# Optimization experiments

Hardware: AMD Instinct MI355X
Metric: run time of the kernel (lower is better)

The kernel has to match this reference:

```python
import jax, jax.numpy as jnp
import numpy as np

N_NODES = 100000
N_EDGES = 2000000


def _init_mlp(key, dims, scale=0.05):
    Ws, bs = [], []
    ks = jax.random.split(key, len(dims) - 1)
    for k, di, do in zip(ks, dims[:-1], dims[1:]):
        Ws.append(jax.random.normal(k, (di, do), dtype=jnp.float32) * scale)
        bs.append(jnp.zeros((do,), dtype=jnp.float32))
    return Ws, bs


def setup_inputs() -> dict:
    key = jax.random.key(0)
    ks = jax.random.split(key, 7)
    d = {
        "t": jax.random.uniform(ks[0], (1,), dtype=jnp.float32),
        "x": jax.random.normal(ks[1], (N_NODES, 4), dtype=jnp.float32),
        "Ofixed": jax.random.normal(ks[2], (N_NODES, 2), dtype=jnp.float32),
        "src_idx": jax.random.randint(ks[3], (N_EDGES,), 0, N_NODES, dtype=jnp.int32),
        "tgt_idx": jax.random.randint(ks[4], (N_EDGES,), 0, N_NODES, dtype=jnp.int32),
    }
    # fR: (2*d_O+1)=13 -> [150]*4 -> 50 ; fO: 50 -> [100] -> 4
    R_Ws, R_bs = _init_mlp(ks[5], [13, 150, 150, 150, 150, 50])
    O_Ws, O_bs = _init_mlp(ks[6], [50, 100, 4])
    for i, (W, b) in enumerate(zip(R_Ws, R_bs)):
        d[f"fR_W{i}"] = W
        d[f"fR_b{i}"] = b
    for i, (W, b) in enumerate(zip(O_Ws, O_bs)):
        d[f"fO_W{i}"] = W
        d[f"fO_b{i}"] = b
    return d


def _mlp(h, Ws, bs):
    # hidden layers with ReLU, linear output (matches MLP in the torch code)
    for W, b in zip(Ws[:-1], bs[:-1]):
        h = jax.nn.relu(h @ W + b)
    return h @ Ws[-1] + bs[-1]


def reference(t, x, Ofixed, src_idx, tgt_idx,
              fR_W0, fR_b0, fR_W1, fR_b1, fR_W2, fR_b2, fR_W3, fR_b3, fR_W4, fR_b4,
              fO_W0, fO_b0, fO_W1, fO_b1):
    O = jnp.concatenate([x, Ofixed], axis=1)            # [N, d_O]
    # Msrc.T @ O and Mtgt.T @ O with 0/1 incidence matrices == gathers
    Rsrc = O[src_idx]                                   # [M, d_O]
    Rtgt = O[tgt_idx]                                   # [M, d_O]
    tt = jnp.broadcast_to(t.reshape(1, 1).astype(O.dtype), (src_idx.shape[0], 1))
    R_prime = jnp.concatenate([Rsrc, Rtgt, tt], axis=1)  # [M, 2*d_O+1]
    E = _mlp(R_prime, [fR_W0, fR_W1, fR_W2, fR_W3, fR_W4],
             [fR_b0, fR_b1, fR_b2, fR_b3, fR_b4])        # [M, d_E]
    # Mtgt @ E == scatter-add of edge messages onto target nodes
    E_prime = jax.ops.segment_sum(E, tgt_idx, num_segments=x.shape[0])  # [N, d_E]
    P = _mlp(E_prime, [fO_W0, fO_W1], [fO_b0, fO_b1])    # [N, d_P]
    return P
```

## Files before the change

kernel.cpp:

```cpp
#include <hip/hip_runtime.h>
#include <hip/hip_bf16.h>

typedef unsigned short u16;
typedef __attribute__((ext_vector_type(8))) short short8;
typedef __attribute__((ext_vector_type(4))) float f32x4;

constexpr int SA     = 168;
constexpr int BLK_E  = 64;
constexpr int NTHR   = 256;
constexpr int CHUNK  = 512;
constexpr int WSLOT  = 50 * CHUNK;
constexpr size_t WT_BYTES = 5ull * WSLOT * 2;
constexpr size_t WS_HDR   = 262144;

constexpr int Ls (int s) { return s == 0 ? 0 : (s <= 15 ? 1 + (s - 1) / 5 : 4); }
constexpr int Kss(int s) { return s == 0 ? 0 : (s <= 15 ? (s - 1) % 5 : s - 16); }

__device__ __forceinline__ u16 f2bf(float f) {
    union { float f; unsigned u; } c; c.f = f;
    return (u16)((c.u + 0x7fffu + ((c.u >> 16) & 1u)) >> 16);
}
__device__ __forceinline__ unsigned pk_bf16(float a, float b) {
    float2 f; f.x = a; f.y = b;
    __hip_bfloat162 h = __float22bfloat162_rn(f);
    return *(unsigned*)&h;
}

__device__ __forceinline__ int kperm(int kp) {
    if (kp < 64)  return (kp & 3) * 16 + (kp >> 2);
    if (kp < 128) { const int m = kp - 64; return (5 + (m & 3)) * 16 + (m >> 2); }
    if (kp < 144) return 4 * 16 + (kp - 128);
    if (kp < 160) return 9 * 16 + (kp - 144);
    return 1 << 30;
}

__global__ void prep_all(const float* __restrict__ W0, const float* __restrict__ W1,
                         const float* __restrict__ W2, const float* __restrict__ W3,
                         const float* __restrict__ W4,
                         const float* __restrict__ B0, const float* __restrict__ B1,
                         const float* __restrict__ B2, const float* __restrict__ B3,
                         const float* __restrict__ B4,
                         u16* __restrict__ Wt)
{
    const int l = blockIdx.y;
    const float* W; const float* B; int DI, DO; bool perm;
    if      (l == 0) { W = W0; B = B0; DI = 13;  DO = 150; perm = false; }
    else if (l == 1) { W = W1; B = B1; DI = 150; DO = 150; perm = true;  }
    else if (l == 2) { W = W2; B = B2; DI = 150; DO = 150; perm = true;  }
    else if (l == 3) { W = W3; B = B3; DI = 150; DO = 150; perm = true;  }
    else             { W = W4; B = B4; DI = 150; DO = 50;  perm = true;  }
    const int kbias = (l == 0) ? 13 : 150;
    u16* dst = Wt + (size_t)l * WSLOT;
    for (int idx = blockIdx.x * blockDim.x + threadIdx.x; idx < WSLOT;
         idx += gridDim.x * blockDim.x) {
        const int chunk = idx / CHUNK;
        const int within = idx - chunk * CHUNK;
        const int lane = within >> 3, e = within & 7;
        const int ks = chunk / 10, j = chunk - ks * 10;
        const int c = lane & 15, q = lane >> 4;
        const int n = j * 16 + c;
        const int kphys = ks * 32 + q * 8 + e;
        const int klog = perm ? kperm(kphys) : kphys;
        float v = 0.f;
        if (n < DO) {
            if (klog < DI)          v = W[klog * DO + n];
            else if (klog == kbias) v = B[n];
        }
        dst[idx] = f2bf(v);
    }
}

__device__ __forceinline__ void loadB(const u16* __restrict__ Wt, int s,
                                      int ng, int lane, short8 (&slot)[5])
{
    const int l = Ls(s), ks = Kss(s);
    const int jb = (l < 4) ? ng * 5 : 0;
    const int nt = (l < 4) ? 5 : 4;
    const u16* base = Wt + (size_t)l * WSLOT + (size_t)(ks * 10 + jb) * CHUNK + lane * 8;
#pragma unroll
    for (int jj = 0; jj < 5; ++jj)
        if (jj < nt) slot[jj] = *(const short8*)&base[jj * CHUNK];
}

__device__ __forceinline__ void epilogue(u16* act, int mg, int ng, int col, int quad,
                                         f32x4 (&acc)[2][5])
{
#pragma unroll
    for (int mtl = 0; mtl < 2; ++mtl)
#pragma unroll
        for (int r = 0; r < 4; ++r) {
            u16* row = &act[((mg * 2 + mtl) * 16 + quad * 4 + r) * SA];
            uint2 pk;
            pk.x = pk_bf16(fmaxf(acc[mtl][0][r], 0.f), fmaxf(acc[mtl][1][r], 0.f));
            pk.y = pk_bf16(fmaxf(acc[mtl][2][r], 0.f), fmaxf(acc[mtl][3][r], 0.f));
            *(uint2*)&row[ng * 64 + col * 4] = pk;
            u16 sv = (u16)pk_bf16(fmaxf(acc[mtl][4][r], 0.f), 0.f);
            if (ng == 1 && col == 6) sv = 0x3F80;
            row[128 + ng * 16 + col] = sv;
        }
}

__global__ __launch_bounds__(NTHR, 4) void edge_kernel(
    const float* __restrict__ t, const float* __restrict__ x, const float* __restrict__ Ofx,
    const int* __restrict__ src, const int* __restrict__ tgt,
    const u16* __restrict__ Wt,
    float* __restrict__ Ep, int n_edges, int copy_mask, size_t copy_elems)
{
    __shared__ __align__(16) u16 act[BLK_E * SA];
    __shared__ int tgt_s[BLK_E];

    const int tid  = threadIdx.x;
    const int lane = tid & 63;
    const int wv   = tid >> 6;
    const int mg   = wv >> 1;
    const int ng   = wv & 1;
    const int col  = lane & 15;
    const int quad = lane >> 4;

    const int xcd = (int)(__builtin_amdgcn_s_getreg(6164) & 7u) & copy_mask;
    float* __restrict__ Epc = Ep + (size_t)xcd * copy_elems;

    short8 Bwin[3][5];
    loadB(Wt, 0, ng, lane, Bwin[0]);
    loadB(Wt, 1, ng, lane, Bwin[1]);
    loadB(Wt, 2, ng, lane, Bwin[2]);

    if (tid < BLK_E) {
        const int e = tid;
        const long long ge = (long long)blockIdx.x * BLK_E + e;
        const bool valid = ge < n_edges;
        const int s = valid ? src[ge] : 0;
        const int g = valid ? tgt[ge] : 0;
        const float4 xs = valid ? *(const float4*)&x[(size_t)s * 4] : float4{0, 0, 0, 0};
        const float2 os = valid ? *(const float2*)&Ofx[(size_t)s * 2] : float2{0, 0};
        const float4 xg = valid ? *(const float4*)&x[(size_t)g * 4] : float4{0, 0, 0, 0};
        const float2 og = valid ? *(const float2*)&Ofx[(size_t)g * 2] : float2{0, 0};
        const float tv = valid ? t[0] : 0.f;
        uint4 w0, w1;
        w0.x = pk_bf16(xs.x, xs.y); w0.y = pk_bf16(xs.z, xs.w);
        w0.z = pk_bf16(os.x, os.y); w0.w = pk_bf16(xg.x, xg.y);
        w1.x = pk_bf16(xg.z, xg.w); w1.y = pk_bf16(og.x, og.y);
        w1.z = pk_bf16(tv, 1.0f);   w1.w = 0u;
        u16* row = &act[e * SA];
        *(uint4*)&row[0]  = w0;
        *(uint4*)&row[8]  = w1;
        *(uint4*)&row[16] = uint4{0, 0, 0, 0};
        *(uint4*)&row[24] = uint4{0, 0, 0, 0};
        tgt_s[e] = valid ? g : -1;
    }
    __syncthreads();

    f32x4 acc[2][5];
    short8 Af[2];

#pragma unroll
    for (int mtl = 0; mtl < 2; ++mtl)
#pragma unroll
        for (int jj = 0; jj < 5; ++jj) acc[mtl][jj] = f32x4{0.f, 0.f, 0.f, 0.f};
#pragma unroll
    for (int mtl = 0; mtl < 2; ++mtl)
        Af[mtl] = *(const short8*)&act[((mg * 2 + mtl) * 16 + col) * SA + quad * 8];
#pragma unroll
    for (int jj = 0; jj < 5; ++jj)
#pragma unroll
        for (int mtl = 0; mtl < 2; ++mtl)
            acc[mtl][jj] = __builtin_amdgcn_mfma_f32_16x16x32_bf16(
                Af[mtl], Bwin[0][jj], acc[mtl][jj], 0, 0, 0);
    loadB(Wt, 3, ng, lane, Bwin[0]);
    __syncthreads();
    epilogue(act, mg, ng, col, quad, acc);
    __syncthreads();

#pragma unroll
    for (int s = 1; s <= 15; ++s) {
        const int ks = (s - 1) % 5;
        const int slot = s % 3;
        if (ks == 0) {
#pragma unroll
            for (int mtl = 0; mtl < 2; ++mtl)
#pragma unroll
                for (int jj = 0; jj < 5; ++jj) acc[mtl][jj] = f32x4{0.f, 0.f, 0.f, 0.f};
        }
#pragma unroll
        for (int mtl = 0; mtl < 2; ++mtl)
            Af[mtl] = *(const short8*)&act[((mg * 2 + mtl) * 16 + col) * SA
                                           + ks * 32 + quad * 8];
#pragma unroll
        for (int jj = 0; jj < 5; ++jj)
#pragma unroll
            for (int mtl = 0; mtl < 2; ++mtl)
                acc[mtl][jj] = __builtin_amdgcn_mfma_f32_16x16x32_bf16(
                    Af[mtl], Bwin[slot][jj], acc[mtl][jj], 0, 0, 0);
        if (s + 3 <= 20) loadB(Wt, s + 3, ng, lane, Bwin[slot]);
        if (ks == 4) {
            __syncthreads();
            epilogue(act, mg, ng, col, quad, acc);
            __syncthreads();
        }
    }

    const int mt4 = mg * 2 + ng;
    f32x4 acc4[4];
#pragma unroll
    for (int jj = 0; jj < 4; ++jj) acc4[jj] = f32x4{0.f, 0.f, 0.f, 0.f};
#pragma unroll
    for (int s = 16; s <= 20; ++s) {
        const int ks = s - 16;
        const int slot = s % 3;
        const short8 A4 = *(const short8*)&act[(mt4 * 16 + col) * SA
                                               + ks * 32 + quad * 8];
#pragma unroll
        for (int jj = 0; jj < 4; ++jj)
            acc4[jj] = __builtin_amdgcn_mfma_f32_16x16x32_bf16(
                A4, Bwin[slot][jj], acc4[jj], 0, 0, 0);
        if (s + 3 <= 20) loadB(Wt, s + 3, ng, lane, Bwin[slot]);
    }

#pragma unroll
    for (int jj = 0; jj < 4; ++jj) {
        const int n = jj * 16 + col;
        if (n < 50) {
#pragma unroll
            for (int r = 0; r < 4; ++r) {
                const int g = tgt_s[mt4 * 16 + quad * 4 + r];
                if (g >= 0) atomicAdd(&Epc[(size_t)g * 50 + n], acc4[jj][r]);
            }
        }
    }
}

template<int DI, int DO, bool RELU>
__device__ __forceinline__ void mlp_layer_t(
    const float* __restrict__ W, const float* __restrict__ B,
    float (*in)[64], float (*out)[64], int tid)
{
    const int et = tid & 15;
    const int jt = tid >> 4;
    constexpr int NG = (DO + 15) / 16;

    float acc0[NG], acc1[NG], acc2[NG], acc3[NG];
#pragma unroll
    for (int g = 0; g < NG; ++g) {
        const int j = jt + 16 * g;
        const float bb = (j < DO) ? B[j] : 0.f;
        acc0[g] = bb; acc1[g] = bb; acc2[g] = bb; acc3[g] = bb;
    }
    for (int k = 0; k < DI; ++k) {
        const float4 a = *(const float4*)&in[k][et * 4];
#pragma unroll
        for (int g = 0; g < NG; ++g) {
            const int j = jt + 16 * g;
            const float wv = (j < DO) ? W[k * DO + j] : 0.f;
            acc0[g] = fmaf(a.x, wv, acc0[g]);
            acc1[g] = fmaf(a.y, wv, acc1[g]);
            acc2[g] = fmaf(a.z, wv, acc2[g]);
            acc3[g] = fmaf(a.w, wv, acc3[g]);
        }
    }
#pragma unroll
    for (int g = 0; g < NG; ++g) {
        const int j = jt + 16 * g;
        if (j < DO) {
            float4 v; v.x = acc0[g]; v.y = acc1[g]; v.z = acc2[g]; v.w = acc3[g];
            if (RELU) {
                v.x = fmaxf(v.x, 0.f); v.y = fmaxf(v.y, 0.f);
                v.z = fmaxf(v.z, 0.f); v.w = fmaxf(v.w, 0.f);
            }
            *(float4*)&out[j][et * 4] = v;
        }
    }
}

__global__ __launch_bounds__(256, 2) void node_kernel(
    const float* __restrict__ Ep, int ncopies, size_t copy_elems,
    const float* __restrict__ W0, const float* __restrict__ B0,
    const float* __restrict__ W1, const float* __restrict__ B1,
    float* __restrict__ P, int n_nodes)
{
    __shared__ float bufA[104][64];
    __shared__ float bufB[104][64];
    const int tid = threadIdx.x;
    const int n0  = blockIdx.x * 64;

    for (int idx = tid; idx < 64 * 50; idx += 256) {
        const int e = idx / 50;
        const int k = idx - e * 50;
        const int n = n0 + e;
        float s = 0.f;
        if (n < n_nodes) {
            const float* p = &Ep[(size_t)n * 50 + k];
            for (int c = 0; c < ncopies; ++c) s += p[(size_t)c * copy_elems];
        }
        bufA[k][e] = s;
    }
    __syncthreads();
    mlp_layer_t<50, 100, true >(W0, B0, bufA, bufB, tid); __syncthreads();
    mlp_layer_t<100, 4, false>(W1, B1, bufB, bufA, tid); __syncthreads();
    for (int idx = tid; idx < 64 * 4; idx += 256) {
        const int e = idx & 63;
        const int j = idx >> 6;
        const int n = n0 + e;
        if (n < n_nodes) P[(size_t)n * 4 + j] = bufA[j][e];
    }
}

extern "C" void kernel_launch(void* const* d_in, const int* in_sizes, int n_in,
                              void* d_out, int out_size, void* d_ws, size_t ws_size,
                              hipStream_t stream)
{
    const float* t   = (const float*)d_in[0];
    const float* x   = (const float*)d_in[1];
    const float* Ofx = (const float*)d_in[2];
    const int*   src = (const int*)d_in[3];
    const int*   tgt = (const int*)d_in[4];
    const float* W0  = (const float*)d_in[5];  const float* B0 = (const float*)d_in[6];
    const float* W1  = (const float*)d_in[7];  const float* B1 = (const float*)d_in[8];
    const float* W2  = (const float*)d_in[9];  const float* B2 = (const float*)d_in[10];
    const float* W3  = (const float*)d_in[11]; const float* B3 = (const float*)d_in[12];
    const float* W4  = (const float*)d_in[13]; const float* B4 = (const float*)d_in[14];
    const float* OW0 = (const float*)d_in[15]; const float* OB0 = (const float*)d_in[16];
    const float* OW1 = (const float*)d_in[17]; const float* OB1 = (const float*)d_in[18];

    const int n_nodes = in_sizes[1] / 4;
    const int n_edges = in_sizes[3];

    u16*   Wt = (u16*)d_ws;
    float* Ep = (float*)((char*)d_ws + WS_HDR);

    const size_t copy_elems = (size_t)n_nodes * 50;
    const size_t avail = (ws_size > WS_HDR) ? ws_size - WS_HDR : 0;
    int ncopies = 1;
    while (ncopies * 2 <= 2 &&
           (size_t)(ncopies * 2) * copy_elems * sizeof(float) <= avail)
        ncopies *= 2;
    const int copy_mask = ncopies - 1;

    prep_all<<<dim3(32, 5), 256, 0, stream>>>(W0, W1, W2, W3, W4,
                                              B0, B1, B2, B3, B4, Wt);
    hipMemsetAsync(Ep, 0, (size_t)ncopies * copy_elems * sizeof(float), stream);

    edge_kernel<<<(n_edges + BLK_E - 1) / BLK_E, NTHR, 0, stream>>>(
        t, x, Ofx, src, tgt, Wt, Ep, n_edges, copy_mask, copy_elems);

    node_kernel<<<(n_nodes + 63) / 64, 256, 0, stream>>>(
        Ep, ncopies, copy_elems, OW0, OB0, OW1, OB1, (float*)d_out, n_nodes);
}
```

Before: 882.5 us.

## Sort edges by target and aggregate runs before atomic scatter

Builds a counting sort of edges by target node each call (histogram, three-stage scan, permutation) and feeds the permuted src/tgt arrays to the edge kernel. Inside the edge kernel, results are staged in shared memory and consecutive edges with the same target are summed before one atomicAdd per run. This cuts global atomic traffic. It also drops the per-XCD duplicate accumulation buffers. The cost is five extra kernel launches, extra passes over the index arrays, and a serial 32-row reduction done by only 100 threads.

```diff
diff --git a/kernel.cpp b/kernel.cpp
--- a/kernel.cpp
+++ b/kernel.cpp
@@ -2,6 +2,7 @@
 #include <hip/hip_bf16.h>
 
 typedef unsigned short u16;
+typedef unsigned int u32;
 typedef __attribute__((ext_vector_type(8))) short short8;
 typedef __attribute__((ext_vector_type(4))) float f32x4;
 
@@ -10,7 +11,6 @@
 constexpr int NTHR   = 256;
 constexpr int CHUNK  = 512;
 constexpr int WSLOT  = 50 * CHUNK;
-constexpr size_t WT_BYTES = 5ull * WSLOT * 2;
 constexpr size_t WS_HDR   = 262144;
 
 constexpr int Ls (int s) { return s == 0 ? 0 : (s <= 15 ? 1 + (s - 1) / 5 : 4); }
@@ -100,11 +100,78 @@
         }
 }
 
+__global__ void hist_kernel(const int* __restrict__ tgt, u32* __restrict__ cnt,
+                            int n_edges)
+{
+    const int e = blockIdx.x * blockDim.x + threadIdx.x;
+    if (e < n_edges) atomicAdd(&cnt[tgt[e]], 1u);
+}
+
+__global__ void scan1_kernel(const u32* __restrict__ cnt, u32* __restrict__ offs,
+                             u32* __restrict__ bsum, int n)
+{
+    __shared__ u32 s[256];
+    const int i = blockIdx.x * 256 + threadIdx.x;
+    const u32 v = (i < n) ? cnt[i] : 0u;
+    s[threadIdx.x] = v; __syncthreads();
+#pragma unroll
+    for (int d = 1; d < 256; d <<= 1) {
+        const u32 t = (threadIdx.x >= d) ? s[threadIdx.x - d] : 0u;
+        __syncthreads();
+        s[threadIdx.x] += t;
+        __syncthreads();
+    }
+    if (i < n) offs[i] = s[threadIdx.x] - v;
+    if (threadIdx.x == 255) bsum[blockIdx.x] = s[255];
+}
+
+__global__ void scan2_kernel(u32* __restrict__ bsum, int nb)
+{
+    __shared__ u32 s[512];
+    const int i = threadIdx.x;
+    const u32 v = (i < nb) ? bsum[i] : 0u;
+    s[i] = v; __syncthreads();
+#pragma unroll
+    for (int d = 1; d < 512; d <<= 1) {
+        const u32 t = (i >= d) ? s[i - d] : 0u;
+        __syncthreads();
+        s[i] += t;
+        __syncthreads();
+    }
+    if (i < nb) bsum[i] = s[i] - v;
+}
+
+__global__ void scan3_kernel(u32* __restrict__ offs, const u32* __restrict__ bsum,
+                             u32* __restrict__ cursor, int n, int n_edges)
+{
+    const int i = blockIdx.x * 256 + threadIdx.x;
+    if (i < n) {
+        const u32 o = offs[i] + bsum[blockIdx.x];
+        offs[i] = o;
+        cursor[i] = o;
+    }
+    if (blockIdx.x == 0 && threadIdx.x == 0) offs[n] = (u32)n_edges;
+}
+
+__global__ void perm_kernel(const int* __restrict__ src, const int* __restrict__ tgt,
+                            u32* __restrict__ cursor,
+                            int* __restrict__ src_perm, int* __restrict__ tgt_perm,
+                            int n_edges)
+{
+    const int e = blockIdx.x * blockDim.x + threadIdx.x;
+    if (e < n_edges) {
+        const int g = tgt[e];
+        const u32 pos = atomicAdd(&cursor[g], 1u);
+        src_perm[pos] = src[e];
+        tgt_perm[pos] = g;
+    }
+}
+
 __global__ __launch_bounds__(NTHR, 4) void edge_kernel(
     const float* __restrict__ t, const float* __restrict__ x, const float* __restrict__ Ofx,
     const int* __restrict__ src, const int* __restrict__ tgt,
     const u16* __restrict__ Wt,
-    float* __restrict__ Ep, int n_edges, int copy_mask, size_t copy_elems)
+    float* __restrict__ Ep, int n_edges)
 {
     __shared__ __align__(16) u16 act[BLK_E * SA];
     __shared__ int tgt_s[BLK_E];
@@ -116,9 +183,6 @@
     const int ng   = wv & 1;
     const int col  = lane & 15;
     const int quad = lane >> 4;
-
-    const int xcd = (int)(__builtin_amdgcn_s_getreg(6164) & 7u) & copy_mask;
-    float* __restrict__ Epc = Ep + (size_t)xcd * copy_elems;
 
     short8 Bwin[3][5];
     loadB(Wt, 0, ng, lane, Bwin[0]);
@@ -216,16 +280,33 @@
         if (s + 3 <= 20) loadB(Wt, s + 3, ng, lane, Bwin[slot]);
     }
 
+    __syncthreads();
+    float* actF = (float*)act;
 #pragma unroll
     for (int jj = 0; jj < 4; ++jj) {
         const int n = jj * 16 + col;
         if (n < 50) {
 #pragma unroll
-            for (int r = 0; r < 4; ++r) {
-                const int g = tgt_s[mt4 * 16 + quad * 4 + r];
-                if (g >= 0) atomicAdd(&Epc[(size_t)g * 50 + n], acc4[jj][r]);
+            for (int r = 0; r < 4; ++r)
+                actF[(mt4 * 16 + quad * 4 + r) * 52 + n] = acc4[jj][r];
+        }
+    }
+    __syncthreads();
+    if (tid < 100) {
+        const int h = tid / 50;
+        const int c = tid - h * 50;
+        int   cur = tgt_s[h * 32];
+        float a   = 0.f;
+        for (int r = h * 32; r < h * 32 + 32; ++r) {
+            const int   g = tgt_s[r];
+            const float v = actF[r * 52 + c];
+            if (g != cur) {
+                if (cur >= 0) atomicAdd(&Ep[(size_t)cur * 50 + c], a);
+                a = 0.f; cur = g;
             }
-        }
+            a += v;
+        }
+        if (cur >= 0) atomicAdd(&Ep[(size_t)cur * 50 + c], a);
     }
 }
 
@@ -324,24 +405,35 @@
     const int n_nodes = in_sizes[1] / 4;
     const int n_edges = in_sizes[3];
 
-    u16*   Wt = (u16*)d_ws;
-    float* Ep = (float*)((char*)d_ws + WS_HDR);
-
+    auto align256 = [](size_t v) { return (v + 255) & ~(size_t)255; };
+    char* ws = (char*)d_ws;
     const size_t copy_elems = (size_t)n_nodes * 50;
-    const size_t avail = (ws_size > WS_HDR) ? ws_size - WS_HDR : 0;
-    int ncopies = 1;
-    while (ncopies * 2 <= 2 &&
-           (size_t)(ncopies * 2) * copy_elems * sizeof(float) <= avail)
-        ncopies *= 2;
-    const int copy_mask = ncopies - 1;
+    size_t o = 0;
+    u16*   Wt       = (u16*)(ws + o);  o = WS_HDR;
+    float* Ep       = (float*)(ws + o); o = align256(o + copy_elems * sizeof(float));
+    u32*   offs     = (u32*)(ws + o);  o = align256(o + (size_t)(n_nodes + 1) * 4);
+    u32*   cursor   = (u32*)(ws + o);  o = align256(o + (size_t)n_nodes * 4);
+    u32*   bsum     = (u32*)(ws + o);  o = align256(o + 512 * 4);
+    int*   src_perm = (int*)(ws + o);  o = align256(o + (size_t)n_edges * 4);
+    int*   tgt_perm = (int*)(ws + o);  o = align256(o + (size_t)n_edges * 4);
+
+    const int NB  = (n_nodes + 255) / 256;
+    const int EBK = (n_edges + 255) / 256;
 
     prep_all<<<dim3(32, 5), 256, 0, stream>>>(W0, W1, W2, W3, W4,
                                               B0, B1, B2, B3, B4, Wt);
-    hipMemsetAsync(Ep, 0, (size_t)ncopies * copy_elems * sizeof(float), stream);
+    hipMemsetAsync(Ep, 0, copy_elems * sizeof(float), stream);
+    hipMemsetAsync(cursor, 0, (size_t)n_nodes * 4, stream);
+
+    hist_kernel <<<EBK, 256, 0, stream>>>(tgt, cursor, n_edges);
+    scan1_kernel<<<NB, 256, 0, stream>>>(cursor, offs, bsum, n_nodes);
+    scan2_kernel<<<1, 512, 0, stream>>>(bsum, NB);
+    scan3_kernel<<<NB, 256, 0, stream>>>(offs, bsum, cursor, n_nodes, n_edges);
+    perm_kernel <<<EBK, 256, 0, stream>>>(src, tgt, cursor, src_perm, tgt_perm, n_edges);
 
     edge_kernel<<<(n_edges + BLK_E - 1) / BLK_E, NTHR, 0, stream>>>(
-        t, x, Ofx, src, tgt, Wt, Ep, n_edges, copy_mask, copy_elems);
+        t, x, Ofx, src_perm, tgt_perm, Wt, Ep, n_edges);
 
     node_kernel<<<(n_nodes + 63) / 64, 256, 0, stream>>>(
-        Ep, ncopies, copy_elems, OW0, OB0, OW1, OB1, (float*)d_out, n_nodes);
-}
+        Ep, 1, copy_elems, OW0, OB0, OW1, OB1, (float*)d_out, n_nodes);
+}
```

Result: no change. 872.1 us (-1.2%).
